# Optimization experiments

Hardware: AMD Instinct MI355X
Metric: run time of the kernel (lower is better)

Reference implementation:

```python
import jax, jax.numpy as jnp
import numpy as np

SCALE = 1.0 / np.float32(64.0 ** 0.5)  # hardcoded in source, not sqrt(d)


def setup_inputs() -> dict:
    key = jax.random.key(0)
    k1, k2 = jax.random.split(key)
    B, S, D, O = 8, 2048, 768, 768
    x = jax.random.normal(k1, (B, S, D), dtype=jnp.float32)
    kernel = jax.random.normal(k2, (3, D, O), dtype=jnp.float32) * 0.02
    return {"x": x, "kernel": kernel}


def reference(x, kernel):
    # x: [B,S,D], kernel: [3,D,O]
    WQ = jnp.einsum('bsd,do->bso', x, kernel[0])
    WK = jnp.einsum('bsd,do->bso', x, kernel[1])
    WV = jnp.einsum('bsd,do->bso', x, kernel[2])
    QK = jnp.einsum('bqo,bko->bqk', WQ, WK) * SCALE  # [B,S,S]
    A = jax.nn.softmax(QK, axis=-1)
    return jnp.einsum('bqk,bko->bqo', A, WV)  # [B,S,O]
```

## Files before the change

### kernel.cpp

```cpp
#include <hip/hip_runtime.h>

typedef unsigned short u16;
typedef __attribute__((ext_vector_type(8))) short short8;
typedef __attribute__((ext_vector_type(4))) float f32x4;
typedef __attribute__((ext_vector_type(8))) unsigned short ushort8;
typedef __attribute__((ext_vector_type(4))) unsigned short ushort4v;

__device__ __forceinline__ u16 f2bf(float f) {
    unsigned int u = __float_as_uint(f);
    u += 0x7FFFu + ((u >> 16) & 1u);
    return (u16)(u >> 16);
}
__device__ __forceinline__ float bf2f(u16 h) {
    return __uint_as_float(((unsigned int)h) << 16);
}

__device__ __forceinline__ void gld_lds16(const void* g, void* l) {
    __builtin_amdgcn_global_load_lds(
        (const __attribute__((address_space(1))) unsigned int*)g,
        (__attribute__((address_space(3))) unsigned int*)l,
        16, 0, 0);
}

template <int MODE>
__global__ __launch_bounds__(256) void gemm_bt(
    const u16* __restrict__ A, const u16* __restrict__ B,
    void* __restrict__ O0, void* __restrict__ O1, void* __restrict__ O2,
    float alpha)
{
    constexpr int K   = (MODE == 2) ? 2048 : 768;
    constexpr int lda = (MODE == 2) ? 2048 : 768;
    constexpr int ldb = (MODE == 2) ? 2048 : 768;

    __shared__ u16 As[2 * 128 * 32];
    __shared__ u16 Bs[2 * 128 * 32];

    const int f = blockIdx.x;
    const int xcd = f & 7;
    const int u = f >> 3;

    int tm, bn, cn, which = 0;
    long aoff = 0, boff = 0;
    if constexpr (MODE == 0) {
        const int c = u >> 4;
        const int rl = u & 15;
        tm = (xcd * 16 + rl) * 128;
        bn = c * 128;
        which = c / 6;
        cn = (c % 6) * 128;
    } else if constexpr (MODE == 1) {
        const int p = u >> 6, t = u & 63, c = t >> 2, rl = t & 3;
        tm = (p * 4 + rl) * 128;
        bn = cn = c * 128;
        aoff = (long)xcd * 2048 * 768;
        boff = aoff;
    } else {
        const int p = u / 12, t = u % 12, c = t >> 1, rl = t & 1;
        tm = (p * 2 + rl) * 128;
        bn = cn = c * 128;
        aoff = (long)xcd * 2048 * 2048;
        boff = (long)xcd * 768 * 2048;
    }

    const u16* Ab = A + aoff;
    const u16* Bb = B + boff;

    const int tid  = threadIdx.x;
    const int lane = tid & 63;
    const int wave = tid >> 6;
    const int wr = wave >> 1;
    const int wc = wave & 1;

    f32x4 acc[4][4] = {};

    const int swz = ((lane >> 4) ^ ((lane >> 1) & 3)) * 8;
    const u16* a_base = As + (wr * 64 + (lane & 15)) * 32 + swz;
    const u16* b_base = Bs + (wc * 64 + (lane & 15)) * 32 + swz;

    const int s0 = tid, s1 = tid + 256;
    const int r0 = s0 >> 2, kc0 = (s0 & 3) ^ ((r0 >> 1) & 3);
    const int r1 = s1 >> 2, kc1 = (s1 & 3) ^ ((r1 >> 1) & 3);
    const long ar0 = (long)(tm + r0) * lda + kc0 * 8;
    const long ar1 = (long)(tm + r1) * lda + kc1 * 8;
    const long br0 = (long)(bn + r0) * ldb + kc0 * 8;
    const long br1 = (long)(bn + r1) * ldb + kc1 * 8;

#define STAGE(BUF, K0) do { \
    gld_lds16(Ab + ar0 + (K0), (void*)(As + (BUF) + s0 * 8)); \
    gld_lds16(Ab + ar1 + (K0), (void*)(As + (BUF) + s1 * 8)); \
    gld_lds16(Bb + br0 + (K0), (void*)(Bs + (BUF) + s0 * 8)); \
    gld_lds16(Bb + br1 + (K0), (void*)(Bs + (BUF) + s1 * 8)); \
} while (0)

#define COMPUTE(BUF) do { \
    short8 a[4], b[4]; \
    _Pragma("unroll") \
    for (int i = 0; i < 4; ++i) a[i] = *(const short8*)(a_base + (BUF) + i * 16 * 32); \
    _Pragma("unroll") \
    for (int j = 0; j < 4; ++j) b[j] = *(const short8*)(b_base + (BUF) + j * 16 * 32); \
    _Pragma("unroll") \
    for (int i = 0; i < 4; ++i) \
    _Pragma("unroll") \
        for (int j = 0; j < 4; ++j) \
            acc[i][j] = __builtin_amdgcn_mfma_f32_16x16x32_bf16( \
                a[i], b[j], acc[i][j], 0, 0, 0); \
} while (0)

    STAGE(0, 0);
    __syncthreads();

#pragma unroll 1
    for (int k0 = 0; k0 < K; k0 += 64) {
        STAGE(4096, k0 + 32);
        COMPUTE(0);
        __syncthreads();
        if (k0 + 64 < K) STAGE(0, k0 + 64);
        COMPUTE(4096);
        __syncthreads();
    }

#undef STAGE
#undef COMPUTE

#pragma unroll
    for (int i = 0; i < 4; ++i) {
        const int row0 = tm + wr * 64 + i * 16 + ((lane >> 4) << 2);
#pragma unroll
        for (int j = 0; j < 4; ++j) {
            const int col = cn + wc * 64 + j * 16 + (lane & 15);
#pragma unroll
            for (int r = 0; r < 4; ++r) {
                const int row = row0 + r;
                const float val = acc[i][j][r] * alpha;
                if constexpr (MODE == 0) {
                    if (which == 0)
                        ((u16*)O0)[(long)row * 768 + col] = f2bf(val);
                    else if (which == 1)
                        ((u16*)O1)[(long)row * 768 + col] = f2bf(val);
                    else
                        ((u16*)O2)[((long)(row >> 11) * 768 + col) * 2048 + (row & 2047)] = f2bf(val);
                } else if constexpr (MODE == 1) {
                    ((u16*)O0)[(long)xcd * 2048 * 2048 + (long)row * 2048 + col] = f2bf(val);
                } else {
                    ((float*)O0)[(long)xcd * 2048 * 768 + (long)row * 768 + col] = val;
                }
            }
        }
    }
}

__global__ __launch_bounds__(256) void cvt_x_kernel(
    const float4* __restrict__ x, ushort4v* __restrict__ out, int n4)
{
    int i = blockIdx.x * 256 + threadIdx.x;
    if (i < n4) {
        float4 f = x[i];
        ushort4v o;
        o.x = f2bf(f.x); o.y = f2bf(f.y); o.z = f2bf(f.z); o.w = f2bf(f.w);
        out[i] = o;
    }
}

__global__ __launch_bounds__(256) void cvt_w_kernel(
    const float* __restrict__ w, u16* __restrict__ wt)
{
    int i = blockIdx.x * 256 + threadIdx.x;
    int d = i % 768;
    int o = (i / 768) % 768;
    int m = i / (768 * 768);
    wt[i] = f2bf(w[((long)m * 768 + d) * 768 + o]);
}

__global__ __launch_bounds__(256) void softmax_kernel(u16* __restrict__ S)
{
    const long row = blockIdx.x;
    u16* p = S + row * 2048;
    const int t = threadIdx.x;
    const int lane = t & 63;
    const int wave = t >> 6;
    __shared__ float red[8];

    ushort8 raw = *(const ushort8*)(p + t * 8);
    float v[8];
    float m = -1e30f;
#pragma unroll
    for (int i = 0; i < 8; ++i) { v[i] = bf2f(raw[i]); m = fmaxf(m, v[i]); }
#pragma unroll
    for (int off = 1; off < 64; off <<= 1) m = fmaxf(m, __shfl_xor(m, off, 64));
    if (lane == 0) red[wave] = m;
    __syncthreads();
    m = fmaxf(fmaxf(red[0], red[1]), fmaxf(red[2], red[3]));

    float s = 0.f;
#pragma unroll
    for (int i = 0; i < 8; ++i) { v[i] = __expf(v[i] - m); s += v[i]; }
#pragma unroll
    for (int off = 1; off < 64; off <<= 1) s += __shfl_xor(s, off, 64);
    if (lane == 0) red[4 + wave] = s;
    __syncthreads();
    s = (red[4] + red[5]) + (red[6] + red[7]);

    const float inv = 1.0f / s;
    ushort8 out;
#pragma unroll
    for (int i = 0; i < 8; ++i) out[i] = f2bf(v[i] * inv);
    *(ushort8*)(p + t * 8) = out;
}

extern "C" void kernel_launch(void* const* d_in, const int* in_sizes, int n_in,
                              void* d_out, int out_size, void* d_ws, size_t ws_size,
                              hipStream_t stream)
{
    const float* x  = (const float*)d_in[0];
    const float* wk = (const float*)d_in[1];
    float* out = (float*)d_out;

    char* ws = (char*)d_ws;
    u16* xbf = (u16*)(ws);
    u16* wt  = (u16*)(ws + 25165824);
    u16* qbf = (u16*)(ws + 28704768);
    u16* kbf = (u16*)(ws + 53870592);
    u16* vt  = (u16*)(ws + 79036416);
    u16* S   = (u16*)(ws + 104202240);

    cvt_x_kernel<<<dim3(12288), dim3(256), 0, stream>>>(
        (const float4*)x, (ushort4v*)xbf, 3145728);
    cvt_w_kernel<<<dim3(6912), dim3(256), 0, stream>>>(wk, wt);

    gemm_bt<0><<<dim3(2304), dim3(256), 0, stream>>>(
        xbf, wt, qbf, kbf, vt, 1.0f);

    gemm_bt<1><<<dim3(2048), dim3(256), 0, stream>>>(
        qbf, kbf, S, nullptr, nullptr, 0.125f);

    softmax_kernel<<<dim3(16384), dim3(256), 0, stream>>>(S);

    gemm_bt<2><<<dim3(768), dim3(256), 0, stream>>>(
        S, vt, out, nullptr, nullptr, 1.0f);
}
```

Baseline: 364.3 us.

## Triple-buffer GEMM LDS staging with one barrier per k-step and manual waitcnts

Moves the bf16 GEMM main loop from double buffering with two barriers per 64-wide step to a three-slot ring buffer. Each 32-wide k-step now waits on vmcnt for just the slot it is about to read, issues one barrier, prefetches two steps ahead, then computes. LDS fragment reads become inline ds_read_b128 with immediate offsets, followed by an explicit lgkmcnt wait. This is meant to cut barrier stalls and hide global-to-LDS latency better, at the cost of 50% more LDS per block, which may lower occupancy, and fragile hand-written waitcnt and scheduling barriers.

Result: no change. 359.6 us (-1.3%).

```diff
diff --git a/kernel.cpp b/kernel.cpp
--- a/kernel.cpp
+++ b/kernel.cpp
@@ -22,6 +22,14 @@
         16, 0, 0);
 }
 
+#define WAITV(N)  asm volatile("s_waitcnt vmcnt(" #N ")" ::: "memory")
+#define ABAR()    do { asm volatile("s_barrier"); \
+                       __builtin_amdgcn_sched_barrier(0); } while (0)
+#define LGKM0()   do { asm volatile("s_waitcnt lgkmcnt(0)" ::: "memory"); \
+                       __builtin_amdgcn_sched_barrier(0); } while (0)
+#define DSR(dst, base, imm) \
+    asm volatile("ds_read_b128 %0, %1 offset:%2" : "=v"(dst) : "v"(base), "n"(imm))
+
 template <int MODE>
 __global__ __launch_bounds__(256) void gemm_bt(
     const u16* __restrict__ A, const u16* __restrict__ B,
@@ -32,8 +40,8 @@
     constexpr int lda = (MODE == 2) ? 2048 : 768;
     constexpr int ldb = (MODE == 2) ? 2048 : 768;
 
-    __shared__ u16 As[2 * 128 * 32];
-    __shared__ u16 Bs[2 * 128 * 32];
+    __shared__ __align__(16) u16 As[3 * 4096];
+    __shared__ __align__(16) u16 Bs[3 * 4096];
 
     const int f = blockIdx.x;
     const int xcd = f & 7;
@@ -73,31 +81,34 @@
 
     f32x4 acc[4][4] = {};
 
+    const int s0 = tid, s1 = tid + 256;
+    const int r0_ = s0 >> 2, kc0 = (s0 & 3) ^ ((r0_ >> 1) & 3);
+    const int r1_ = s1 >> 2, kc1 = (s1 & 3) ^ ((r1_ >> 1) & 3);
+    const long ar0 = (long)(tm + r0_) * lda + kc0 * 8;
+    const long ar1 = (long)(tm + r1_) * lda + kc1 * 8;
+    const long br0 = (long)(bn + r0_) * ldb + kc0 * 8;
+    const long br1 = (long)(bn + r1_) * ldb + kc1 * 8;
+
+#define STAGE(BO, K0) do { \
+    gld_lds16(Ab + ar0 + (K0), (void*)(As + (BO) + s0 * 8)); \
+    gld_lds16(Ab + ar1 + (K0), (void*)(As + (BO) + s1 * 8)); \
+    gld_lds16(Bb + br0 + (K0), (void*)(Bs + (BO) + s0 * 8)); \
+    gld_lds16(Bb + br1 + (K0), (void*)(Bs + (BO) + s1 * 8)); \
+} while (0)
+
+    const unsigned aLds = (unsigned)(unsigned long long)(&As[0]);
+    const unsigned bLds = (unsigned)(unsigned long long)(&Bs[0]);
     const int swz = ((lane >> 4) ^ ((lane >> 1) & 3)) * 8;
-    const u16* a_base = As + (wr * 64 + (lane & 15)) * 32 + swz;
-    const u16* b_base = Bs + (wc * 64 + (lane & 15)) * 32 + swz;
-
-    const int s0 = tid, s1 = tid + 256;
-    const int r0 = s0 >> 2, kc0 = (s0 & 3) ^ ((r0 >> 1) & 3);
-    const int r1 = s1 >> 2, kc1 = (s1 & 3) ^ ((r1 >> 1) & 3);
-    const long ar0 = (long)(tm + r0) * lda + kc0 * 8;
-    const long ar1 = (long)(tm + r1) * lda + kc1 * 8;
-    const long br0 = (long)(bn + r0) * ldb + kc0 * 8;
-    const long br1 = (long)(bn + r1) * ldb + kc1 * 8;
-
-#define STAGE(BUF, K0) do { \
-    gld_lds16(Ab + ar0 + (K0), (void*)(As + (BUF) + s0 * 8)); \
-    gld_lds16(Ab + ar1 + (K0), (void*)(As + (BUF) + s1 * 8)); \
-    gld_lds16(Bb + br0 + (K0), (void*)(Bs + (BUF) + s0 * 8)); \
-    gld_lds16(Bb + br1 + (K0), (void*)(Bs + (BUF) + s1 * 8)); \
-} while (0)
-
-#define COMPUTE(BUF) do { \
+    const unsigned a_b = aLds + 2u * ((wr * 64 + (lane & 15)) * 32 + swz);
+    const unsigned b_b = bLds + 2u * ((wc * 64 + (lane & 15)) * 32 + swz);
+
+#define COMPUTE(BO) do { \
     short8 a[4], b[4]; \
-    _Pragma("unroll") \
-    for (int i = 0; i < 4; ++i) a[i] = *(const short8*)(a_base + (BUF) + i * 16 * 32); \
-    _Pragma("unroll") \
-    for (int j = 0; j < 4; ++j) b[j] = *(const short8*)(b_base + (BUF) + j * 16 * 32); \
+    DSR(a[0], a_b, (BO) * 2 + 0);    DSR(a[1], a_b, (BO) * 2 + 1024); \
+    DSR(a[2], a_b, (BO) * 2 + 2048); DSR(a[3], a_b, (BO) * 2 + 3072); \
+    DSR(b[0], b_b, (BO) * 2 + 0);    DSR(b[1], b_b, (BO) * 2 + 1024); \
+    DSR(b[2], b_b, (BO) * 2 + 2048); DSR(b[3], b_b, (BO) * 2 + 3072); \
+    LGKM0(); \
     _Pragma("unroll") \
     for (int i = 0; i < 4; ++i) \
     _Pragma("unroll") \
@@ -106,21 +117,29 @@
                 a[i], b[j], acc[i][j], 0, 0, 0); \
 } while (0)
 
+#define ITER(K0, BOC, BON) do { \
+    if ((K0) + 32 < K) { WAITV(4); } else { WAITV(0); } \
+    ABAR(); \
+    if ((K0) + 64 < K) STAGE(BON, (K0) + 64); \
+    COMPUTE(BOC); \
+} while (0)
+
     STAGE(0, 0);
-    __syncthreads();
-
+    STAGE(4096, 32);
+
+    int kb = 0;
 #pragma unroll 1
-    for (int k0 = 0; k0 < K; k0 += 64) {
-        STAGE(4096, k0 + 32);
-        COMPUTE(0);
-        __syncthreads();
-        if (k0 + 64 < K) STAGE(0, k0 + 64);
-        COMPUTE(4096);
-        __syncthreads();
-    }
-
+    for (; kb + 96 <= K; kb += 96) {
+        ITER(kb,      0,    8192);
+        ITER(kb + 32, 4096, 0);
+        ITER(kb + 64, 8192, 4096);
+    }
+    if (kb < K)
+        ITER(kb, 0, 8192);
+
+#undef ITER
+#undef COMPUTE
 #undef STAGE
-#undef COMPUTE
 
 #pragma unroll
     for (int i = 0; i < 4; ++i) {
```
